# Performance work log

Hardware: AMD Instinct MI355X
Metric: run time of the kernel (lower is better)

The kernel has to match this reference:

```python
import jax, jax.numpy as jnp
import numpy as np

EMBED = 2048
T = 2048  # max_seq_length
BATCH = 2  # hardcoded by the module's initial-state shape


def setup_inputs() -> dict:
    key = jax.random.key(0)
    ks = jax.random.split(key, 7)
    s = 0.02
    return {
        "x": jax.random.normal(ks[0], (BATCH, EMBED), dtype=jnp.float32),
        "W_ih": jax.random.normal(ks[1], (4 * EMBED, EMBED), dtype=jnp.float32) * s,
        "W_hh": jax.random.normal(ks[2], (4 * EMBED, EMBED), dtype=jnp.float32) * s,
        "b_ih": jax.random.normal(ks[3], (4 * EMBED,), dtype=jnp.float32) * s,
        "b_hh": jax.random.normal(ks[4], (4 * EMBED,), dtype=jnp.float32) * s,
        "W_out": jax.random.normal(ks[5], (EMBED, EMBED), dtype=jnp.float32) * s,
        "b_out": jax.random.normal(ks[6], (EMBED,), dtype=jnp.float32) * s,
    }


def reference(x, W_ih, W_hh, b_ih, b_hh, W_out, b_out):
    E = x.shape[-1]

    def step(carry, _):
        inp, h, c = carry  # each [B, E]
        gates = inp @ W_ih.T + b_ih + h @ W_hh.T + b_hh  # [B, 4E]
        i, f, g, o = jnp.split(gates, 4, axis=-1)  # PyTorch gate order i,f,g,o
        c_new = jax.nn.sigmoid(f) * c + jax.nn.sigmoid(i) * jnp.tanh(g)
        h_new = jax.nn.sigmoid(o) * jnp.tanh(c_new)
        # output of single-layer LSTM == h_new; it is fed back as next input
        return (h_new, h_new, c_new), h_new

    h0 = jnp.zeros((x.shape[0], E), dtype=x.dtype)
    c0 = jnp.zeros((x.shape[0], E), dtype=x.dtype)
    _, seq = jax.lax.scan(step, (x, h0, c0), None, length=T)  # [T, B, E]

    out = seq @ W_out.T + b_out  # dropout is identity in eval
    return jnp.transpose(out, (1, 0, 2))  # [B, T, E]
```

## Files before the change

### kernel.cpp

```cpp
#include <hip/hip_runtime.h>
#include <hip/hip_fp16.h>
#include <stdint.h>


#define E 2048
#define NBLK 256
#define NTHR 512
#define HLDS_B 2304
#define PLS_STRIDE 20
#define PLS_PAR 640
#define SMEM_MAIN 23680
#define SMEM_PROJ 131072

typedef uint32_t u32;
typedef unsigned long long u64;

__device__ __forceinline__ float sigf(float x){
  return __builtin_amdgcn_rcpf(1.0f + __expf(-x));
}
__device__ __forceinline__ float tanhfast(float x){
  float e = __expf(2.0f * x);
  return 1.0f - 2.0f * __builtin_amdgcn_rcpf(e + 1.0f);
}

#define ROWFMA8(W0, W1, W2, W3, A0, A1) \
  A0 = fmaf(__low2float(W0),  p0.x, A0); A0 = fmaf(__high2float(W0), p0.y, A0); \
  A0 = fmaf(__low2float(W1),  p0.z, A0); A0 = fmaf(__high2float(W1), p0.w, A0); \
  A0 = fmaf(__low2float(W2),  p1.x, A0); A0 = fmaf(__high2float(W2), p1.y, A0); \
  A0 = fmaf(__low2float(W3),  p1.z, A0); A0 = fmaf(__high2float(W3), p1.w, A0); \
  A1 = fmaf(__low2float(W0),  q0.x, A1); A1 = fmaf(__high2float(W0), q0.y, A1); \
  A1 = fmaf(__low2float(W1),  q0.z, A1); A1 = fmaf(__high2float(W1), q0.w, A1); \
  A1 = fmaf(__low2float(W2),  q1.x, A1); A1 = fmaf(__high2float(W2), q1.y, A1); \
  A1 = fmaf(__low2float(W3),  q1.z, A1); A1 = fmaf(__high2float(W3), q1.w, A1);

#define POLLCHK(J, UJ) \
  if (pend & (1 << J)){ \
    if ((u32)(UJ >> 32) == tag){ \
      hlds[cdst[J]] = __uint_as_float((u32)UJ); \
      pend &= ~(1 << J); \
    } \
  }

#define ISSUE8(R0, R1, R2, R3, R4, R5, R6, R7) \
  asm volatile( \
    "global_load_dwordx2 %0, %8, off sc0 sc1\n\t" \
    "global_load_dwordx2 %1, %8, off offset:512 sc0 sc1\n\t" \
    "global_load_dwordx2 %2, %8, off offset:1024 sc0 sc1\n\t" \
    "global_load_dwordx2 %3, %8, off offset:1536 sc0 sc1\n\t" \
    "global_load_dwordx2 %4, %8, off offset:2048 sc0 sc1\n\t" \
    "global_load_dwordx2 %5, %8, off offset:2560 sc0 sc1\n\t" \
    "global_load_dwordx2 %6, %8, off offset:3072 sc0 sc1\n\t" \
    "global_load_dwordx2 %7, %8, off offset:3584 sc0 sc1" \
    : "=&v"(R0), "=&v"(R1), "=&v"(R2), "=&v"(R3), \
      "=&v"(R4), "=&v"(R5), "=&v"(R6), "=&v"(R7) \
    : "v"(src) : "memory")

__global__ void __launch_bounds__(NTHR, 1) lstm_kernel(
    const float* __restrict__ xin, const float* __restrict__ Wih,
    const float* __restrict__ Whh, const float* __restrict__ bih,
    const float* __restrict__ bhh, u64* __restrict__ chk,
    float* __restrict__ seqout)
{
  extern __shared__ char smem[];
  float* hlds = (float*)smem;
  float* pls  = (float*)(smem + 18432);
  float* bias = (float*)(smem + 23552);

  const int tid  = threadIdx.x;
  const int blk  = blockIdx.x;
  const int e0   = blk << 3;
  const int lane = tid & 63;
  const int wv   = tid >> 6;
  const int rg   = lane >> 3;
  const int ksl  = lane & 7;
  const int ks   = (wv << 3) + ksl;
  const int k0   = ks << 5;

  if (tid < 32){
    const int grow = ((tid >> 3) << 11) + e0 + (tid & 7);
    bias[tid] = bih[grow] + bhh[grow];
  }
  for (int i = tid; i < 2 * E; i += NTHR){
    const int b = i >> 11, k = i & 2047;
    hlds[b * HLDS_B + (k >> 5) * 36 + (k & 31)] = xin[i];
  }
  __syncthreads();

  const float* hb0 = hlds + ks * 36;
  const float* hb1 = hlds + HLDS_B + ks * 36;

  __half2 wh[64];
  float acc0[4] = {0.f, 0.f, 0.f, 0.f};
  float acc1[4] = {0.f, 0.f, 0.f, 0.f};
  #pragma unroll
  for (int rr = 0; rr < 4; ++rr){
    const int row  = (rg << 2) + rr;
    const int grow = ((row >> 3) << 11) + e0 + (row & 7);
    const float* pa = Wih + (size_t)grow * E + k0;
    const float* pb = Whh + (size_t)grow * E + k0;
    #pragma unroll
    for (int c = 0; c < 8; ++c){
      float4 a = *(const float4*)(pa + (c << 2));
      float4 b = *(const float4*)(pb + (c << 2));
      wh[(rr << 4) + (c << 1)    ] =
        __halves2half2(__float2half_rn(a.x + b.x), __float2half_rn(a.y + b.y));
      wh[(rr << 4) + (c << 1) + 1] =
        __halves2half2(__float2half_rn(a.z + b.z), __float2half_rn(a.w + b.w));
      float4 x0 = *(const float4*)(hb0 + (c << 2));
      float4 x1 = *(const float4*)(hb1 + (c << 2));
      acc0[rr] = fmaf(a.x, x0.x, acc0[rr]); acc0[rr] = fmaf(a.y, x0.y, acc0[rr]);
      acc0[rr] = fmaf(a.z, x0.z, acc0[rr]); acc0[rr] = fmaf(a.w, x0.w, acc0[rr]);
      acc1[rr] = fmaf(a.x, x1.x, acc1[rr]); acc1[rr] = fmaf(a.y, x1.y, acc1[rr]);
      acc1[rr] = fmaf(a.z, x1.z, acc1[rr]); acc1[rr] = fmaf(a.w, x1.w, acc1[rr]);
    }
  }

  const float br = bias[lane & 31];
  float creg = 0.0f;

  int cdst[8];
  #pragma unroll
  for (int j = 0; j < 8; ++j){
    const int c = (wv << 9) + (j << 6) + lane;
    const int b = (c >> 3) & 1;
    const int e = ((c >> 4) << 3) | (c & 7);
    cdst[j] = b * HLDS_B + (e >> 5) * 36 + (e & 31);
  }
  u64* const pchk0 = chk;
  u64* const pchk1 = chk + 4096;

  for (int t = 0; t < 2048; ++t){
    #pragma unroll
    for (int m = 1; m <= 4; m <<= 1){
      #pragma unroll
      for (int rr = 0; rr < 4; ++rr){
        acc0[rr] += __shfl_xor(acc0[rr], m, 64);
        acc1[rr] += __shfl_xor(acc1[rr], m, 64);
      }
    }
    if (ksl == 0){
      float2* pw = (float2*)(pls + (t & 1) * PLS_PAR);
      #pragma unroll
      for (int rr = 0; rr < 4; ++rr)
        pw[((rg << 2) + rr) * (PLS_STRIDE / 2) + wv] = make_float2(acc0[rr], acc1[rr]);
    }
    __syncthreads();

    if (wv == 0){
      const int r = lane & 31;
      const int b = lane >> 5;
      const float* rp = pls + (t & 1) * PLS_PAR + r * PLS_STRIDE;
      float4 v0 = *(const float4*)(rp);
      float4 v1 = *(const float4*)(rp + 4);
      float4 v2 = *(const float4*)(rp + 8);
      float4 v3 = *(const float4*)(rp + 12);
      float s = br + (b ? (v0.y + v0.w + v1.y + v1.w + v2.y + v2.w + v3.y + v3.w)
                        : (v0.x + v0.z + v1.x + v1.z + v2.x + v2.z + v3.x + v3.z));
      const float gi = s;
      const float gf = __shfl(s, (lane + 8)  & 63, 64);
      const float gg = __shfl(s, (lane + 16) & 63, 64);
      const float go = __shfl(s, (lane + 24) & 63, 64);
      if (r < 8){
        const float cn = sigf(gf) * creg + sigf(gi) * tanhfast(gg);
        const float hn = sigf(go) * tanhfast(cn);
        creg = cn;
        if (t < 2047){
          const u64 pk = ((u64)(u32)(t + 1) << 32) | (u64)__float_as_uint(hn);
          u64* dst = (((t + 1) & 1) ? pchk1 : pchk0) + (blk << 4) + (b << 3) + r;
          asm volatile("global_store_dwordx2 %0, %1, off sc0 sc1"
                       :: "v"(dst), "v"(pk) : "memory");
        }
        seqout[(((size_t)b << 11) + (size_t)t) * E + e0 + r] = hn;
      }
    }
    if (t == 2047) break;

    {
      const u64* src = (((t + 1) & 1) ? pchk1 : pchk0) + (wv << 9) + lane;
      const u32 tag = (u32)(t + 1);
      u64 a0_, a1_, a2_, a3_, a4_, a5_, a6_, a7_;
      u64 b0_, b1_, b2_, b3_, b4_, b5_, b6_, b7_;
      ISSUE8(a0_, a1_, a2_, a3_, a4_, a5_, a6_, a7_);
      ISSUE8(b0_, b1_, b2_, b3_, b4_, b5_, b6_, b7_);
      int pend = 0xFF;
      for (;;){
        asm volatile("s_waitcnt vmcnt(8)" ::: "memory");
        POLLCHK(0, a0_) POLLCHK(1, a1_) POLLCHK(2, a2_) POLLCHK(3, a3_)
        POLLCHK(4, a4_) POLLCHK(5, a5_) POLLCHK(6, a6_) POLLCHK(7, a7_)
        if (!pend) break;
        ISSUE8(a0_, a1_, a2_, a3_, a4_, a5_, a6_, a7_);
        asm volatile("s_waitcnt vmcnt(8)" ::: "memory");
        POLLCHK(0, b0_) POLLCHK(1, b1_) POLLCHK(2, b2_) POLLCHK(3, b3_)
        POLLCHK(4, b4_) POLLCHK(5, b5_) POLLCHK(6, b6_) POLLCHK(7, b7_)
        if (!pend) break;
        ISSUE8(b0_, b1_, b2_, b3_, b4_, b5_, b6_, b7_);
      }
      asm volatile("s_waitcnt vmcnt(0)"
        :: "v"(a0_), "v"(a1_), "v"(a2_), "v"(a3_),
           "v"(a4_), "v"(a5_), "v"(a6_), "v"(a7_),
           "v"(b0_), "v"(b1_), "v"(b2_), "v"(b3_),
           "v"(b4_), "v"(b5_), "v"(b6_), "v"(b7_) : "memory");
      asm volatile("s_waitcnt lgkmcnt(0)" ::: "memory");
      __builtin_amdgcn_sched_barrier(0);
    }

    #pragma unroll
    for (int rr = 0; rr < 4; ++rr){ acc0[rr] = 0.f; acc1[rr] = 0.f; }
    #pragma unroll
    for (int c8 = 0; c8 < 4; ++c8){
      float4 p0 = *(const float4*)(hb0 + (c8 << 3));
      float4 p1 = *(const float4*)(hb0 + (c8 << 3) + 4);
      float4 q0 = *(const float4*)(hb1 + (c8 << 3));
      float4 q1 = *(const float4*)(hb1 + (c8 << 3) + 4);
      #pragma unroll
      for (int rr = 0; rr < 4; ++rr){
        ROWFMA8(wh[(rr << 4) + (c8 << 2)],     wh[(rr << 4) + (c8 << 2) + 1],
                wh[(rr << 4) + (c8 << 2) + 2], wh[(rr << 4) + (c8 << 2) + 3],
                acc0[rr], acc1[rr]);
      }
    }
  }
}

__global__ void __launch_bounds__(256, 1) proj_kernel(
    float* __restrict__ io, const float* __restrict__ Wout,
    const float* __restrict__ bout)
{
  extern __shared__ char smem[];
  float* alds = (float*)smem;
  const int tid = threadIdx.x;
  const size_t rbase = (size_t)blockIdx.x * 16 * E;

  for (int idx = tid; idx < 8192; idx += 256){
    float4 v = *(const float4*)(io + rbase + ((size_t)idx << 2));
    *(float4*)(alds + (idx << 2)) = v;
  }
  __syncthreads();

  for (int p = 0; p < 4; ++p){
    const int n0 = (p << 8) + tid;
    const int n1 = n0 + 1024;
    const float* wr0 = Wout + (size_t)n0 * E;
    const float* wr1 = Wout + (size_t)n1 * E;
    float acc0[16], acc1[16];
    #pragma unroll
    for (int m = 0; m < 16; ++m){ acc0[m] = 0.0f; acc1[m] = 0.0f; }
    for (int kc = 0; kc < 256; ++kc){
      const float4 a0v = *(const float4*)(wr0 + (kc << 3));
      const float4 a1v = *(const float4*)(wr0 + (kc << 3) + 4);
      const float4 b0v = *(const float4*)(wr1 + (kc << 3));
      const float4 b1v = *(const float4*)(wr1 + (kc << 3) + 4);
      const float* ap = alds + (kc << 3);
      #pragma unroll
      for (int m = 0; m < 16; ++m){
        const float* a = ap + (m << 11);
        float4 x0 = *(const float4*)(a);
        float4 x1 = *(const float4*)(a + 4);
        acc0[m] = fmaf(a0v.x, x0.x, acc0[m]); acc0[m] = fmaf(a0v.y, x0.y, acc0[m]);
        acc0[m] = fmaf(a0v.z, x0.z, acc0[m]); acc0[m] = fmaf(a0v.w, x0.w, acc0[m]);
        acc0[m] = fmaf(a1v.x, x1.x, acc0[m]); acc0[m] = fmaf(a1v.y, x1.y, acc0[m]);
        acc0[m] = fmaf(a1v.z, x1.z, acc0[m]); acc0[m] = fmaf(a1v.w, x1.w, acc0[m]);
        acc1[m] = fmaf(b0v.x, x0.x, acc1[m]); acc1[m] = fmaf(b0v.y, x0.y, acc1[m]);
        acc1[m] = fmaf(b0v.z, x0.z, acc1[m]); acc1[m] = fmaf(b0v.w, x0.w, acc1[m]);
        acc1[m] = fmaf(b1v.x, x1.x, acc1[m]); acc1[m] = fmaf(b1v.y, x1.y, acc1[m]);
        acc1[m] = fmaf(b1v.z, x1.z, acc1[m]); acc1[m] = fmaf(b1v.w, x1.w, acc1[m]);
      }
    }
    const float bo0 = bout[n0];
    const float bo1 = bout[n1];
    #pragma unroll
    for (int m = 0; m < 16; ++m){
      io[rbase + ((size_t)m << 11) + n0] = acc0[m] + bo0;
      io[rbase + ((size_t)m << 11) + n1] = acc1[m] + bo1;
    }
  }
}

extern "C" void kernel_launch(void* const* d_in, const int* in_sizes, int n_in,
                              void* d_out, int out_size, void* d_ws, size_t ws_size,
                              hipStream_t stream)
{
  const float* xin  = (const float*)d_in[0];
  const float* Wih  = (const float*)d_in[1];
  const float* Whh  = (const float*)d_in[2];
  const float* bih  = (const float*)d_in[3];
  const float* bhh  = (const float*)d_in[4];
  const float* Wout = (const float*)d_in[5];
  const float* bout = (const float*)d_in[6];
  float* out = (float*)d_out;

  u64* chk = (u64*)d_ws;

  hipFuncSetAttribute((const void*)lstm_kernel,
                      hipFuncAttributeMaxDynamicSharedMemorySize, SMEM_MAIN);
  hipFuncSetAttribute((const void*)proj_kernel,
                      hipFuncAttributeMaxDynamicSharedMemorySize, SMEM_PROJ);

  void* args[] = { (void*)&xin, (void*)&Wih, (void*)&Whh, (void*)&bih, (void*)&bhh,
                   (void*)&chk, (void*)&out };
  hipLaunchCooperativeKernel((const void*)lstm_kernel, dim3(NBLK), dim3(NTHR),
                             args, SMEM_MAIN, stream);

  proj_kernel<<<256, 256, SMEM_PROJ, stream>>>(out, Wout, bout);
}
```

Baseline: 9.502 ms.

## Parallelize gate epilogue across all waves, simplify polling, and retile projection with fp16 LDS

Spreads the gate reduction and cell update so every wave handles one hidden unit, replacing the single-wave epilogue with shuffle reductions and a sigmoid-based tanh for the g gate. Bias is now read straight from global memory instead of staged in LDS. The double-buffered spin-poll on neighbour checkpoints becomes one batch of loads with s_sleep and selective reloads of still-pending entries, trading fewer outstanding loads for possibly longer wake-up latency. The projection kernel moves to 512 threads with 32 rows per block and keeps activations in LDS as fp16, halving LDS traffic per row at some precision cost.

```diff
diff --git a/kernel.cpp b/kernel.cpp
--- a/kernel.cpp
+++ b/kernel.cpp
@@ -7,9 +7,8 @@
 #define NBLK 256
 #define NTHR 512
 #define HLDS_B 2304
-#define PLS_STRIDE 20
-#define PLS_PAR 640
-#define SMEM_MAIN 23680
+#define PLS_PAR 576
+#define SMEM_MAIN 23040
 #define SMEM_PROJ 131072
 
 typedef uint32_t u32;
@@ -55,6 +54,12 @@
       "=&v"(R4), "=&v"(R5), "=&v"(R6), "=&v"(R7) \
     : "v"(src) : "memory")
 
+#define RELOAD(J, UJ, OFS) \
+  if (pend & (1 << J)){ \
+    asm volatile("global_load_dwordx2 %0, %1, off offset:" OFS " sc0 sc1" \
+                 : "=v"(UJ) : "v"(src) : "memory"); \
+  }
+
 __global__ void __launch_bounds__(NTHR, 1) lstm_kernel(
     const float* __restrict__ xin, const float* __restrict__ Wih,
     const float* __restrict__ Whh, const float* __restrict__ bih,
@@ -64,7 +69,6 @@
   extern __shared__ char smem[];
   float* hlds = (float*)smem;
   float* pls  = (float*)(smem + 18432);
-  float* bias = (float*)(smem + 23552);
 
   const int tid  = threadIdx.x;
   const int blk  = blockIdx.x;
@@ -76,10 +80,6 @@
   const int ks   = (wv << 3) + ksl;
   const int k0   = ks << 5;
 
-  if (tid < 32){
-    const int grow = ((tid >> 3) << 11) + e0 + (tid & 7);
-    bias[tid] = bih[grow] + bhh[grow];
-  }
   for (int i = tid; i < 2 * E; i += NTHR){
     const int b = i >> 11, k = i & 2047;
     hlds[b * HLDS_B + (k >> 5) * 36 + (k & 31)] = xin[i];
@@ -115,7 +115,11 @@
     }
   }
 
-  const float br = bias[lane & 31];
+  const int g  = lane >> 4;
+  const int bb = (lane >> 3) & 1;
+  const int w  = lane & 7;
+  const size_t growt = ((size_t)g << 11) + e0 + wv;
+  const float br = bih[growt] + bhh[growt];
   float creg = 0.0f;
 
   int cdst[8];
@@ -139,38 +143,37 @@
       }
     }
     if (ksl == 0){
-      float2* pw = (float2*)(pls + (t & 1) * PLS_PAR);
+      float* pw = pls + (t & 1) * PLS_PAR;
       #pragma unroll
       for (int rr = 0; rr < 4; ++rr)
-        pw[((rg << 2) + rr) * (PLS_STRIDE / 2) + wv] = make_float2(acc0[rr], acc1[rr]);
+        *(float2*)(pw + ((rg << 2) + rr) * 18 + (wv << 1)) =
+          make_float2(acc0[rr], acc1[rr]);
     }
     __syncthreads();
 
-    if (wv == 0){
-      const int r = lane & 31;
-      const int b = lane >> 5;
-      const float* rp = pls + (t & 1) * PLS_PAR + r * PLS_STRIDE;
-      float4 v0 = *(const float4*)(rp);
-      float4 v1 = *(const float4*)(rp + 4);
-      float4 v2 = *(const float4*)(rp + 8);
-      float4 v3 = *(const float4*)(rp + 12);
-      float s = br + (b ? (v0.y + v0.w + v1.y + v1.w + v2.y + v2.w + v3.y + v3.w)
-                        : (v0.x + v0.z + v1.x + v1.z + v2.x + v2.z + v3.x + v3.z));
-      const float gi = s;
-      const float gf = __shfl(s, (lane + 8)  & 63, 64);
-      const float gg = __shfl(s, (lane + 16) & 63, 64);
-      const float go = __shfl(s, (lane + 24) & 63, 64);
-      if (r < 8){
-        const float cn = sigf(gf) * creg + sigf(gi) * tanhfast(gg);
-        const float hn = sigf(go) * tanhfast(cn);
-        creg = cn;
+    {
+      float s = pls[(t & 1) * PLS_PAR + ((g << 3) + wv) * 18 + (w << 1) + bb];
+      s += __shfl_xor(s, 1, 64);
+      s += __shfl_xor(s, 2, 64);
+      s += __shfl_xor(s, 4, 64);
+      s += br;
+      const float arg = (g == 2) ? (s + s) : s;
+      const float t0v = sigf(arg);
+      const float nl = (g == 2) ? (2.0f * t0v - 1.0f) : t0v;
+      const float SI = __shfl(nl, (lane + 48) & 63, 64);
+      const float TG = __shfl(nl, (lane + 16) & 63, 64);
+      const float SO = __shfl(nl, (lane + 32) & 63, 64);
+      const float cn = nl * creg + SI * TG;
+      const float hn = SO * tanhfast(cn);
+      creg = cn;
+      if (g == 1 && w == 0){
         if (t < 2047){
           const u64 pk = ((u64)(u32)(t + 1) << 32) | (u64)__float_as_uint(hn);
-          u64* dst = (((t + 1) & 1) ? pchk1 : pchk0) + (blk << 4) + (b << 3) + r;
+          u64* dst = (((t + 1) & 1) ? pchk1 : pchk0) + (blk << 4) + (bb << 3) + wv;
           asm volatile("global_store_dwordx2 %0, %1, off sc0 sc1"
                        :: "v"(dst), "v"(pk) : "memory");
         }
-        seqout[(((size_t)b << 11) + (size_t)t) * E + e0 + r] = hn;
+        seqout[(((size_t)bb << 11) + (size_t)t) * E + e0 + wv] = hn;
       }
     }
     if (t == 2047) break;
@@ -179,27 +182,20 @@
       const u64* src = (((t + 1) & 1) ? pchk1 : pchk0) + (wv << 9) + lane;
       const u32 tag = (u32)(t + 1);
       u64 a0_, a1_, a2_, a3_, a4_, a5_, a6_, a7_;
-      u64 b0_, b1_, b2_, b3_, b4_, b5_, b6_, b7_;
       ISSUE8(a0_, a1_, a2_, a3_, a4_, a5_, a6_, a7_);
-      ISSUE8(b0_, b1_, b2_, b3_, b4_, b5_, b6_, b7_);
+      asm volatile("s_waitcnt vmcnt(0)" ::: "memory");
       int pend = 0xFF;
-      for (;;){
-        asm volatile("s_waitcnt vmcnt(8)" ::: "memory");
+      while (true){
         POLLCHK(0, a0_) POLLCHK(1, a1_) POLLCHK(2, a2_) POLLCHK(3, a3_)
         POLLCHK(4, a4_) POLLCHK(5, a5_) POLLCHK(6, a6_) POLLCHK(7, a7_)
-        if (!pend) break;
-        ISSUE8(a0_, a1_, a2_, a3_, a4_, a5_, a6_, a7_);
-        asm volatile("s_waitcnt vmcnt(8)" ::: "memory");
-        POLLCHK(0, b0_) POLLCHK(1, b1_) POLLCHK(2, b2_) POLLCHK(3, b3_)
-        POLLCHK(4, b4_) POLLCHK(5, b5_) POLLCHK(6, b6_) POLLCHK(7, b7_)
-        if (!pend) break;
-        ISSUE8(b0_, b1_, b2_, b3_, b4_, b5_, b6_, b7_);
-      }
-      asm volatile("s_waitcnt vmcnt(0)"
-        :: "v"(a0_), "v"(a1_), "v"(a2_), "v"(a3_),
-           "v"(a4_), "v"(a5_), "v"(a6_), "v"(a7_),
-           "v"(b0_), "v"(b1_), "v"(b2_), "v"(b3_),
-           "v"(b4_), "v"(b5_), "v"(b6_), "v"(b7_) : "memory");
+        if (pend == 0) break;
+        __builtin_amdgcn_s_sleep(1);
+        RELOAD(0, a0_, "0")    RELOAD(1, a1_, "512")
+        RELOAD(2, a2_, "1024") RELOAD(3, a3_, "1536")
+        RELOAD(4, a4_, "2048") RELOAD(5, a5_, "2560")
+        RELOAD(6, a6_, "3072") RELOAD(7, a7_, "3584")
+        asm volatile("s_waitcnt vmcnt(0)" ::: "memory");
+      }
       asm volatile("s_waitcnt lgkmcnt(0)" ::: "memory");
       __builtin_amdgcn_sched_barrier(0);
     }
@@ -222,54 +218,65 @@
   }
 }
 
-__global__ void __launch_bounds__(256, 1) proj_kernel(
+__global__ void __launch_bounds__(512, 1) proj_kernel(
     float* __restrict__ io, const float* __restrict__ Wout,
     const float* __restrict__ bout)
 {
   extern __shared__ char smem[];
-  float* alds = (float*)smem;
+  u32* ah = (u32*)smem;
   const int tid = threadIdx.x;
-  const size_t rbase = (size_t)blockIdx.x * 16 * E;
-
-  for (int idx = tid; idx < 8192; idx += 256){
-    float4 v = *(const float4*)(io + rbase + ((size_t)idx << 2));
-    *(float4*)(alds + (idx << 2)) = v;
+  const size_t rbase = (size_t)blockIdx.x * 32 * E;
+
+  for (int idx = tid; idx < 32768; idx += 512){
+    const float2 v = *(const float2*)(io + rbase + ((size_t)idx << 1));
+    ah[idx] = (u32)__half_as_ushort(__float2half_rn(v.x))
+            | ((u32)__half_as_ushort(__float2half_rn(v.y)) << 16);
   }
   __syncthreads();
 
-  for (int p = 0; p < 4; ++p){
-    const int n0 = (p << 8) + tid;
+  for (int p = 0; p < 2; ++p){
+    const int n0 = (p << 9) + tid;
     const int n1 = n0 + 1024;
     const float* wr0 = Wout + (size_t)n0 * E;
     const float* wr1 = Wout + (size_t)n1 * E;
-    float acc0[16], acc1[16];
-    #pragma unroll
-    for (int m = 0; m < 16; ++m){ acc0[m] = 0.0f; acc1[m] = 0.0f; }
+    float acc0[32], acc1[32];
+    #pragma unroll
+    for (int m = 0; m < 32; ++m){ acc0[m] = 0.0f; acc1[m] = 0.0f; }
     for (int kc = 0; kc < 256; ++kc){
       const float4 a0v = *(const float4*)(wr0 + (kc << 3));
       const float4 a1v = *(const float4*)(wr0 + (kc << 3) + 4);
       const float4 b0v = *(const float4*)(wr1 + (kc << 3));
       const float4 b1v = *(const float4*)(wr1 + (kc << 3) + 4);
-      const float* ap = alds + (kc << 3);
+      const u32* hp = ah + (kc << 2);
       #pragma unroll
-      for (int m = 0; m < 16; ++m){
-        const float* a = ap + (m << 11);
-        float4 x0 = *(const float4*)(a);
-        float4 x1 = *(const float4*)(a + 4);
-        acc0[m] = fmaf(a0v.x, x0.x, acc0[m]); acc0[m] = fmaf(a0v.y, x0.y, acc0[m]);
-        acc0[m] = fmaf(a0v.z, x0.z, acc0[m]); acc0[m] = fmaf(a0v.w, x0.w, acc0[m]);
-        acc0[m] = fmaf(a1v.x, x1.x, acc0[m]); acc0[m] = fmaf(a1v.y, x1.y, acc0[m]);
-        acc0[m] = fmaf(a1v.z, x1.z, acc0[m]); acc0[m] = fmaf(a1v.w, x1.w, acc0[m]);
-        acc1[m] = fmaf(b0v.x, x0.x, acc1[m]); acc1[m] = fmaf(b0v.y, x0.y, acc1[m]);
-        acc1[m] = fmaf(b0v.z, x0.z, acc1[m]); acc1[m] = fmaf(b0v.w, x0.w, acc1[m]);
-        acc1[m] = fmaf(b1v.x, x1.x, acc1[m]); acc1[m] = fmaf(b1v.y, x1.y, acc1[m]);
-        acc1[m] = fmaf(b1v.z, x1.z, acc1[m]); acc1[m] = fmaf(b1v.w, x1.w, acc1[m]);
+      for (int m = 0; m < 32; ++m){
+        const uint4 hv = *(const uint4*)(hp + (m << 10));
+        const __half2 h0 = __builtin_bit_cast(__half2, hv.x);
+        const __half2 h1 = __builtin_bit_cast(__half2, hv.y);
+        const __half2 h2 = __builtin_bit_cast(__half2, hv.z);
+        const __half2 h3 = __builtin_bit_cast(__half2, hv.w);
+        acc0[m] = fmaf(a0v.x, __low2float(h0),  acc0[m]);
+        acc0[m] = fmaf(a0v.y, __high2float(h0), acc0[m]);
+        acc0[m] = fmaf(a0v.z, __low2float(h1),  acc0[m]);
+        acc0[m] = fmaf(a0v.w, __high2float(h1), acc0[m]);
+        acc0[m] = fmaf(a1v.x, __low2float(h2),  acc0[m]);
+        acc0[m] = fmaf(a1v.y, __high2float(h2), acc0[m]);
+        acc0[m] = fmaf(a1v.z, __low2float(h3),  acc0[m]);
+        acc0[m] = fmaf(a1v.w, __high2float(h3), acc0[m]);
+        acc1[m] = fmaf(b0v.x, __low2float(h0),  acc1[m]);
+        acc1[m] = fmaf(b0v.y, __high2float(h0), acc1[m]);
+        acc1[m] = fmaf(b0v.z, __low2float(h1),  acc1[m]);
+        acc1[m] = fmaf(b0v.w, __high2float(h1), acc1[m]);
+        acc1[m] = fmaf(b1v.x, __low2float(h2),  acc1[m]);
+        acc1[m] = fmaf(b1v.y, __high2float(h2), acc1[m]);
+        acc1[m] = fmaf(b1v.z, __low2float(h3),  acc1[m]);
+        acc1[m] = fmaf(b1v.w, __high2float(h3), acc1[m]);
       }
     }
     const float bo0 = bout[n0];
     const float bo1 = bout[n1];
     #pragma unroll
-    for (int m = 0; m < 16; ++m){
+    for (int m = 0; m < 32; ++m){
       io[rbase + ((size_t)m << 11) + n0] = acc0[m] + bo0;
       io[rbase + ((size_t)m << 11) + n1] = acc1[m] + bo1;
     }
@@ -301,5 +308,5 @@
   hipLaunchCooperativeKernel((const void*)lstm_kernel, dim3(NBLK), dim3(NTHR),
                              args, SMEM_MAIN, stream);
 
-  proj_kernel<<<256, 256, SMEM_PROJ, stream>>>(out, Wout, bout);
-}
+  proj_kernel<<<128, 512, SMEM_PROJ, stream>>>(out, Wout, bout);
+}
```

Result: slower. 12.89 ms (+35.6%).
